# Performance work log

Hardware: AMD Instinct MI355X
Metric: run time of the kernel (lower is better)

Reference implementation:

```python
import jax, jax.numpy as jnp
import numpy as np

N_NODES = 100000
N_EDGES = 1000000
N_LABEL = 200000
D_IN = 64
D_HID = 64


def setup_inputs() -> dict:
    key = jax.random.key(0)
    ks = jax.random.split(key, 9)
    s = 1.0 / np.sqrt(D_IN)
    return {
        "x": jax.random.normal(ks[0], (N_NODES, D_IN), jnp.float32),
        "edge_index": jax.random.randint(ks[1], (2, N_EDGES), 0, N_NODES, jnp.int64),
        "edge_label_index": jax.random.randint(ks[2], (2, N_LABEL), 0, N_NODES, jnp.int64),
        "W1_l": jax.random.normal(ks[3], (D_IN, D_HID), jnp.float32) * s,
        "W1_r": jax.random.normal(ks[4], (D_IN, D_HID), jnp.float32) * s,
        "b1": jnp.zeros((D_HID,), jnp.float32),
        "W2_l": jax.random.normal(ks[5], (D_HID, D_HID), jnp.float32) * s,
        "W2_r": jax.random.normal(ks[6], (D_HID, D_HID), jnp.float32) * s,
        "b2": jnp.zeros((D_HID,), jnp.float32),
    }


def _sage_conv(x, edge_index, W_l, W_r, b):
    # PyG SAGEConv with mean aggregation: out = mean_agg @ W_l + b + x @ W_r
    src, dst = edge_index[0], edge_index[1]
    n = x.shape[0]
    # gather source features, scatter-sum into destination nodes
    agg = jax.ops.segment_sum(x[src], dst, num_segments=n)          # [N, D]
    cnt = jax.ops.segment_sum(jnp.ones(src.shape, x.dtype), dst, num_segments=n)
    mean = agg / jnp.maximum(cnt, 1.0)[:, None]
    return mean @ W_l + x @ W_r + b


def reference(x, edge_index, edge_label_index, W1_l, W1_r, b1, W2_l, W2_r, b2):
    h = jax.nn.relu(_sage_conv(x, edge_index, W1_l, W1_r, b1))
    z = _sage_conv(h, edge_index, W2_l, W2_r, b2)
    # dot-product edge decode
    src_e = z[edge_label_index[0]]  # [E_label, D]
    dst_e = z[edge_label_index[1]]
    return jnp.sum(src_e * dst_e, axis=-1)  # [E_label]
```

## Files before the change

### kernel.cpp

```cpp
#include <hip/hip_runtime.h>

#define D 64
#define NB_SHIFT 9
#define NODES_PER_B 512
#define CAP1 12288

typedef __attribute__((ext_vector_type(8))) short short8;
typedef __attribute__((ext_vector_type(4))) float f32x4;

__device__ inline unsigned short f2bf(float f) {
    unsigned int u = __float_as_uint(f);
    return (unsigned short)((u + 0x7FFFu + ((u >> 16) & 1u)) >> 16);
}
__device__ inline float bf2f(unsigned short s) {
    return __uint_as_float(((unsigned int)s) << 16);
}

__global__ void f32_to_bf16_kernel(const float* __restrict__ in,
                                   unsigned short* __restrict__ outp, int n4) {
    int i = blockIdx.x * blockDim.x + threadIdx.x;
    int stride = gridDim.x * blockDim.x;
    for (int t = i; t < n4; t += stride) {
        float4 v = ((const float4*)in)[t];
        ushort4 o;
        o.x = f2bf(v.x); o.y = f2bf(v.y); o.z = f2bf(v.z); o.w = f2bf(v.w);
        ((ushort4*)outp)[t] = o;
    }
}

__global__ __launch_bounds__(256) void bin_edges_kernel(
        const int* __restrict__ src, const int* __restrict__ dst,
        int* __restrict__ gcount, int2* __restrict__ binned,
        int n_edges, int n_buckets) {
    __shared__ int lhist[256];
    __shared__ int lbase[256];
    int tid = threadIdx.x;
    int per = (n_edges + gridDim.x - 1) / gridDim.x;
    int beg = blockIdx.x * per;
    int end = min(beg + per, n_edges);

    lhist[tid] = 0;
    __syncthreads();
    for (int e = beg + tid; e < end; e += 256)
        atomicAdd(&lhist[dst[e] >> NB_SHIFT], 1);
    __syncthreads();
    if (tid < n_buckets && lhist[tid] > 0)
        lbase[tid] = atomicAdd(&gcount[tid], lhist[tid]);
    else
        lbase[tid] = 0;
    __syncthreads();
    lhist[tid] = 0;
    __syncthreads();
    for (int e = beg + tid; e < end; e += 256) {
        int d = dst[e];
        int b = d >> NB_SHIFT;
        int off = lbase[b] + atomicAdd(&lhist[b], 1);
        if (off < CAP1)
            binned[(size_t)b * CAP1 + off] = make_int2(src[e], d);
    }
}

__global__ __launch_bounds__(256) void bucket_scan_kernel(
        const int* __restrict__ gcount, int* __restrict__ gbase,
        int* __restrict__ rowp, int n_buckets, int n_nodes, int n_edges) {
    __shared__ int tmp[256];
    int tid = threadIdx.x;
    int v = (tid < n_buckets) ? min(gcount[tid], CAP1) : 0;
    tmp[tid] = v;
    __syncthreads();
    for (int off = 1; off < 256; off <<= 1) {
        int t = 0;
        if (tid >= off) t = tmp[tid - off];
        __syncthreads();
        if (tid >= off) tmp[tid] += t;
        __syncthreads();
    }
    if (tid < n_buckets) gbase[tid] = tmp[tid] - v;
    if (tid == 0) rowp[n_nodes] = n_edges;
}

__global__ __launch_bounds__(256) void build_csr_kernel(
        const int2* __restrict__ binned, const int* __restrict__ gcount,
        const int* __restrict__ gbase, int* __restrict__ rowp,
        int* __restrict__ ssrc, int n_nodes) {
    __shared__ int lhist[NODES_PER_B];
    __shared__ int lbase[NODES_PER_B];
    __shared__ int tmp[256];
    __shared__ int stage[CAP1];

    int b        = blockIdx.x;
    int tid      = threadIdx.x;
    int nodebase = b << NB_SHIFT;
    int nlocal   = min(NODES_PER_B, n_nodes - nodebase);
    int cnt      = min(gcount[b], CAP1);
    int base     = gbase[b];
    const int2* ebuf = binned + (size_t)b * CAP1;

    lhist[tid] = 0;
    lhist[tid + 256] = 0;
    __syncthreads();
    for (int i = tid; i < cnt; i += 256)
        atomicAdd(&lhist[ebuf[i].y - nodebase], 1);
    __syncthreads();

    int a0 = lhist[2 * tid];
    int a1 = lhist[2 * tid + 1];
    tmp[tid] = a0 + a1;
    __syncthreads();
    for (int off = 1; off < 256; off <<= 1) {
        int t = 0;
        if (tid >= off) t = tmp[tid - off];
        __syncthreads();
        if (tid >= off) tmp[tid] += t;
        __syncthreads();
    }
    int excl = tmp[tid] - (a0 + a1);
    lbase[2 * tid]     = excl;
    lbase[2 * tid + 1] = excl + a0;
    __syncthreads();

    for (int j = tid; j < nlocal; j += 256)
        rowp[nodebase + j] = base + lbase[j];

    lhist[tid] = 0;
    lhist[tid + 256] = 0;
    __syncthreads();

    for (int i = tid; i < cnt; i += 256) {
        int2 e = ebuf[i];
        int ln = e.y - nodebase;
        int off = atomicAdd(&lhist[ln], 1);
        stage[lbase[ln] + off] = e.x;
    }
    __syncthreads();

    for (int i = tid; i < cnt; i += 256)
        ssrc[base + i] = stage[i];
}

__global__ void pack_w4_kernel(const float* __restrict__ W0,
                               const float* __restrict__ W1,
                               const float* __restrict__ W2,
                               const float* __restrict__ W3,
                               unsigned short* __restrict__ pw) {
    int idx = blockIdx.x * blockDim.x + threadIdx.x;
    if (idx >= 4 * 4096) return;
    int m = idx >> 12;
    int r = idx & 4095;
    const float* W = (m == 0) ? W0 : (m == 1) ? W1 : (m == 2) ? W2 : W3;
    int j    = r & 7;
    int lane = (r >> 3) & 63;
    int kk   = (r >> 9) & 1;
    int ct   = r >> 10;
    int k    = kk * 32 + ((lane >> 4) & 3) * 8 + j;
    int col  = ct * 16 + (lane & 15);
    pw[idx] = f2bf(W[k * D + col]);
}

__global__ __launch_bounds__(256) void aggregate_bf16_kernel(
        const unsigned short* __restrict__ feat,
        const int* __restrict__ row_ptr,
        const int* __restrict__ sorted_src,
        unsigned short* __restrict__ mean_out,
        int n_nodes) {
    int lane = threadIdx.x & 63;
    int r    = lane >> 4;
    int c    = lane & 15;
    int wave   = (int)((blockIdx.x * blockDim.x + threadIdx.x) >> 6);
    int nwaves = (int)((gridDim.x * blockDim.x) >> 6);

    for (int node = wave; node < n_nodes; node += nwaves) {
        int beg = row_ptr[node];
        int end = row_ptr[node + 1];
        int endm1 = end - 1;
        float a0 = 0.f, a1 = 0.f, a2 = 0.f, a3 = 0.f;

        for (int i = beg; i < end; i += 8) {
            int e0 = i + r;
            int e1 = i + 4 + r;
            int s0 = sorted_src[min(e0, endm1)];
            int s1 = sorted_src[min(e1, endm1)];
            ushort4 v0 = *(const ushort4*)(feat + ((size_t)s0 << 6) + (c << 2));
            ushort4 v1 = *(const ushort4*)(feat + ((size_t)s1 << 6) + (c << 2));
            if (e0 < end) {
                a0 += bf2f(v0.x); a1 += bf2f(v0.y);
                a2 += bf2f(v0.z); a3 += bf2f(v0.w);
            }
            if (e1 < end) {
                a0 += bf2f(v1.x); a1 += bf2f(v1.y);
                a2 += bf2f(v1.z); a3 += bf2f(v1.w);
            }
        }
        a0 += __shfl_xor(a0, 16); a1 += __shfl_xor(a1, 16);
        a2 += __shfl_xor(a2, 16); a3 += __shfl_xor(a3, 16);
        a0 += __shfl_xor(a0, 32); a1 += __shfl_xor(a1, 32);
        a2 += __shfl_xor(a2, 32); a3 += __shfl_xor(a3, 32);

        float inv = 1.0f / (float)max(end - beg, 1);
        if (r == 0) {
            ushort4 o;
            o.x = f2bf(a0 * inv); o.y = f2bf(a1 * inv);
            o.z = f2bf(a2 * inv); o.w = f2bf(a3 * inv);
            *(ushort4*)(mean_out + ((size_t)node << 6) + (c << 2)) = o;
        }
    }
}

__global__ __launch_bounds__(256) void sage_linear_mfma_kernel(
        const unsigned short* __restrict__ mean,
        const unsigned short* __restrict__ xin,
        const unsigned short* __restrict__ pwl,
        const unsigned short* __restrict__ pwr,
        const float* __restrict__ bias,
        unsigned short* __restrict__ outp,
        int n_nodes, int do_relu) {
    int lane = threadIdx.x & 63;
    int wid  = threadIdx.x >> 6;
    int arow = lane & 15;
    int kgrp = lane >> 4;

    short8 wl[4][2], wr[4][2];
#pragma unroll
    for (int ct = 0; ct < 4; ++ct)
#pragma unroll
        for (int kk = 0; kk < 2; ++kk) {
            wl[ct][kk] = *(const short8*)(pwl + (((ct * 2 + kk) * 64 + lane) << 3));
            wr[ct][kk] = *(const short8*)(pwr + (((ct * 2 + kk) * 64 + lane) << 3));
        }
    float bj[4];
#pragma unroll
    for (int ct = 0; ct < 4; ++ct) bj[ct] = bias[ct * 16 + arow];

    int wave   = blockIdx.x * 4 + wid;
    int nwaves = gridDim.x * 4;
    int ntiles = (n_nodes + 15) >> 4;

    for (int t = wave; t < ntiles; t += nwaves) {
        int base = t * 16;
        int lrow = base + arow;
        if (lrow >= n_nodes) lrow = n_nodes - 1;
        const unsigned short* mrow = mean + (size_t)lrow * D + kgrp * 8;
        const unsigned short* xrow = xin  + (size_t)lrow * D + kgrp * 8;
        short8 am0 = *(const short8*)(mrow);
        short8 am1 = *(const short8*)(mrow + 32);
        short8 ax0 = *(const short8*)(xrow);
        short8 ax1 = *(const short8*)(xrow + 32);

#pragma unroll
        for (int ct = 0; ct < 4; ++ct) {
            f32x4 acc = {0.f, 0.f, 0.f, 0.f};
            acc = __builtin_amdgcn_mfma_f32_16x16x32_bf16(am0, wl[ct][0], acc, 0, 0, 0);
            acc = __builtin_amdgcn_mfma_f32_16x16x32_bf16(am1, wl[ct][1], acc, 0, 0, 0);
            acc = __builtin_amdgcn_mfma_f32_16x16x32_bf16(ax0, wr[ct][0], acc, 0, 0, 0);
            acc = __builtin_amdgcn_mfma_f32_16x16x32_bf16(ax1, wr[ct][1], acc, 0, 0, 0);
            int col = ct * 16 + arow;
#pragma unroll
            for (int rr = 0; rr < 4; ++rr) {
                int row = base + kgrp * 4 + rr;
                float v = acc[rr] + bj[ct];
                if (do_relu) v = fmaxf(v, 0.0f);
                if (row < n_nodes) outp[(size_t)row * D + col] = f2bf(v);
            }
        }
    }
}

__global__ __launch_bounds__(256) void decode_bf16_kernel(
        const unsigned short* __restrict__ z,
        const int* __restrict__ esrc,
        const int* __restrict__ edst,
        float* __restrict__ out,
        int n) {
    int lane = threadIdx.x & 63;
    int g    = lane >> 4;
    int c    = lane & 15;
    int wave   = (int)((blockIdx.x * blockDim.x + threadIdx.x) >> 6);
    int nwaves = (int)((gridDim.x * blockDim.x) >> 6);
    int niter  = (n + 3) >> 2;

    for (int it = wave; it < niter; it += nwaves) {
        int e  = it * 4 + g;
        int ec = min(e, n - 1);
        int s  = esrc[ec];
        int d0 = edst[ec];
        ushort4 vs = *(const ushort4*)(z + ((size_t)s  << 6) + (c << 2));
        ushort4 vd = *(const ushort4*)(z + ((size_t)d0 << 6) + (c << 2));
        float p = bf2f(vs.x) * bf2f(vd.x) + bf2f(vs.y) * bf2f(vd.y) +
                  bf2f(vs.z) * bf2f(vd.z) + bf2f(vs.w) * bf2f(vd.w);
        p += __shfl_xor(p, 1);
        p += __shfl_xor(p, 2);
        p += __shfl_xor(p, 4);
        p += __shfl_xor(p, 8);
        if (c == 0 && e < n) out[e] = p;
    }
}

extern "C" void kernel_launch(void* const* d_in, const int* in_sizes, int n_in,
                              void* d_out, int out_size, void* d_ws, size_t ws_size,
                              hipStream_t stream) {
    const float* x   = (const float*)d_in[0];
    const int*   ei  = (const int*)d_in[1];
    const int*   eli = (const int*)d_in[2];
    const float* W1l = (const float*)d_in[3];
    const float* W1r = (const float*)d_in[4];
    const float* b1  = (const float*)d_in[5];
    const float* W2l = (const float*)d_in[6];
    const float* W2r = (const float*)d_in[7];
    const float* b2  = (const float*)d_in[8];
    float* out = (float*)d_out;

    const int n_nodes = in_sizes[0] / D;
    const int n_edges = in_sizes[1] / 2;
    const int n_label = in_sizes[2] / 2;
    const int n_buckets = (n_nodes + NODES_PER_B - 1) >> NB_SHIFT;

    const int* e_src = ei;
    const int* e_dst = ei + n_edges;
    const int* l_src = eli;
    const int* l_dst = eli + n_label;

    unsigned short* xb    = (unsigned short*)d_ws;
    unsigned short* meanb = xb + (size_t)n_nodes * D;
    unsigned short* h     = meanb + (size_t)n_nodes * D;
    unsigned short* z     = h + (size_t)n_nodes * D;
    int* rowp   = (int*)(z + (size_t)n_nodes * D);
    int* ssrc   = rowp + (n_nodes + 1);
    int* gcount = ssrc + n_edges + 8;
    int* gbase  = gcount + 256;
    unsigned short* pw = (unsigned short*)(gbase + 256);
    unsigned short* pw1l = pw;
    unsigned short* pw1r = pw + 4096;
    unsigned short* pw2l = pw + 8192;
    unsigned short* pw2r = pw + 12288;
    int2* binned = (int2*)h;

    dim3 blk(256);
    dim3 grd_nodes(2048);
    dim3 grd_linear(512);

    f32_to_bf16_kernel<<<grd_nodes, blk, 0, stream>>>(x, xb, n_nodes * D / 4);
    pack_w4_kernel<<<dim3(64), blk, 0, stream>>>(W1l, W1r, W2l, W2r, pw);

    hipMemsetAsync(gcount, 0, 256 * sizeof(int), stream);
    bin_edges_kernel<<<dim3(512), blk, 0, stream>>>(e_src, e_dst, gcount, binned,
                                                    n_edges, n_buckets);
    bucket_scan_kernel<<<dim3(1), blk, 0, stream>>>(gcount, gbase, rowp,
                                                    n_buckets, n_nodes, n_edges);
    build_csr_kernel<<<dim3(n_buckets), blk, 0, stream>>>(binned, gcount, gbase,
                                                          rowp, ssrc, n_nodes);

    aggregate_bf16_kernel<<<grd_nodes, blk, 0, stream>>>(xb, rowp, ssrc, meanb, n_nodes);
    sage_linear_mfma_kernel<<<grd_linear, blk, 0, stream>>>(meanb, xb, pw1l, pw1r, b1,
                                                            h, n_nodes, 1);

    aggregate_bf16_kernel<<<grd_nodes, blk, 0, stream>>>(h, rowp, ssrc, meanb, n_nodes);
    sage_linear_mfma_kernel<<<grd_linear, blk, 0, stream>>>(meanb, h, pw2l, pw2r, b2,
                                                            z, n_nodes, 0);

    decode_bf16_kernel<<<grd_nodes, blk, 0, stream>>>(z, l_src, l_dst, out, n_label);
}
```

Measured before the change: 156.4 us.

## Pack binned edges into one int, fuse bucket scan, contiguous node ranges in aggregation

Binned edges are stored as a single int (source shifted left, plus the local destination offset) instead of an int2, which halves the binning traffic. The single-block bucket scan kernel is folded into build_csr, where every block recomputes the prefix over bucket counts, removing one launch and the gbase buffer. The aggregation kernel now gives each wave a contiguous range of nodes so row_ptr is read once per node, and it unrolls the edge loop to 16 edges per iteration for more loads in flight. The packing assumes the shifted source index fits in 32 bits, and contiguous node ranges can leave waves unevenly loaded.

```diff
diff --git a/kernel.cpp b/kernel.cpp
--- a/kernel.cpp
+++ b/kernel.cpp
@@ -30,7 +30,7 @@
 
 __global__ __launch_bounds__(256) void bin_edges_kernel(
         const int* __restrict__ src, const int* __restrict__ dst,
-        int* __restrict__ gcount, int2* __restrict__ binned,
+        int* __restrict__ gcount, int* __restrict__ binned,
         int n_edges, int n_buckets) {
     __shared__ int lhist[256];
     __shared__ int lbase[256];
@@ -56,15 +56,23 @@
         int b = d >> NB_SHIFT;
         int off = lbase[b] + atomicAdd(&lhist[b], 1);
         if (off < CAP1)
-            binned[(size_t)b * CAP1 + off] = make_int2(src[e], d);
-    }
-}
-
-__global__ __launch_bounds__(256) void bucket_scan_kernel(
-        const int* __restrict__ gcount, int* __restrict__ gbase,
-        int* __restrict__ rowp, int n_buckets, int n_nodes, int n_edges) {
+            binned[(size_t)b * CAP1 + off] =
+                (src[e] << NB_SHIFT) | (d & (NODES_PER_B - 1));
+    }
+}
+
+__global__ __launch_bounds__(256) void build_csr_kernel(
+        const int* __restrict__ binned, const int* __restrict__ gcount,
+        int* __restrict__ rowp, int* __restrict__ ssrc,
+        int n_nodes, int n_buckets, int n_edges) {
+    __shared__ int lhist[NODES_PER_B];
+    __shared__ int lbase[NODES_PER_B];
     __shared__ int tmp[256];
+    __shared__ int stage[CAP1];
+
+    int b   = blockIdx.x;
     int tid = threadIdx.x;
+
     int v = (tid < n_buckets) ? min(gcount[tid], CAP1) : 0;
     tmp[tid] = v;
     __syncthreads();
@@ -75,32 +83,20 @@
         if (tid >= off) tmp[tid] += t;
         __syncthreads();
     }
-    if (tid < n_buckets) gbase[tid] = tmp[tid] - v;
-    if (tid == 0) rowp[n_nodes] = n_edges;
-}
-
-__global__ __launch_bounds__(256) void build_csr_kernel(
-        const int2* __restrict__ binned, const int* __restrict__ gcount,
-        const int* __restrict__ gbase, int* __restrict__ rowp,
-        int* __restrict__ ssrc, int n_nodes) {
-    __shared__ int lhist[NODES_PER_B];
-    __shared__ int lbase[NODES_PER_B];
-    __shared__ int tmp[256];
-    __shared__ int stage[CAP1];
-
-    int b        = blockIdx.x;
-    int tid      = threadIdx.x;
+    int base = (b == 0) ? 0 : tmp[b - 1];
+    int cnt  = min(gcount[b], CAP1);
+    if (b == 0 && tid == 0) rowp[n_nodes] = n_edges;
+    __syncthreads();
+
     int nodebase = b << NB_SHIFT;
     int nlocal   = min(NODES_PER_B, n_nodes - nodebase);
-    int cnt      = min(gcount[b], CAP1);
-    int base     = gbase[b];
-    const int2* ebuf = binned + (size_t)b * CAP1;
+    const int* ebuf = binned + (size_t)b * CAP1;
 
     lhist[tid] = 0;
     lhist[tid + 256] = 0;
     __syncthreads();
     for (int i = tid; i < cnt; i += 256)
-        atomicAdd(&lhist[ebuf[i].y - nodebase], 1);
+        atomicAdd(&lhist[ebuf[i] & (NODES_PER_B - 1)], 1);
     __syncthreads();
 
     int a0 = lhist[2 * tid];
@@ -127,10 +123,10 @@
     __syncthreads();
 
     for (int i = tid; i < cnt; i += 256) {
-        int2 e = ebuf[i];
-        int ln = e.y - nodebase;
+        int e  = ebuf[i];
+        int ln = e & (NODES_PER_B - 1);
         int off = atomicAdd(&lhist[ln], 1);
-        stage[lbase[ln] + off] = e.x;
+        stage[lbase[ln] + off] = e >> NB_SHIFT;
     }
     __syncthreads();
 
@@ -168,20 +164,27 @@
     int c    = lane & 15;
     int wave   = (int)((blockIdx.x * blockDim.x + threadIdx.x) >> 6);
     int nwaves = (int)((gridDim.x * blockDim.x) >> 6);
-
-    for (int node = wave; node < n_nodes; node += nwaves) {
-        int beg = row_ptr[node];
+    int npw  = (n_nodes + nwaves - 1) / nwaves;
+    int nbeg = wave * npw;
+    int nend = min(nbeg + npw, n_nodes);
+    if (nbeg >= nend) return;
+
+    int beg = row_ptr[nbeg];
+    for (int node = nbeg; node < nend; ++node) {
         int end = row_ptr[node + 1];
         int endm1 = end - 1;
         float a0 = 0.f, a1 = 0.f, a2 = 0.f, a3 = 0.f;
 
-        for (int i = beg; i < end; i += 8) {
-            int e0 = i + r;
-            int e1 = i + 4 + r;
+        for (int i = beg; i < end; i += 16) {
+            int e0 = i + r, e1 = i + 4 + r, e2 = i + 8 + r, e3 = i + 12 + r;
             int s0 = sorted_src[min(e0, endm1)];
             int s1 = sorted_src[min(e1, endm1)];
+            int s2 = sorted_src[min(e2, endm1)];
+            int s3 = sorted_src[min(e3, endm1)];
             ushort4 v0 = *(const ushort4*)(feat + ((size_t)s0 << 6) + (c << 2));
             ushort4 v1 = *(const ushort4*)(feat + ((size_t)s1 << 6) + (c << 2));
+            ushort4 v2 = *(const ushort4*)(feat + ((size_t)s2 << 6) + (c << 2));
+            ushort4 v3 = *(const ushort4*)(feat + ((size_t)s3 << 6) + (c << 2));
             if (e0 < end) {
                 a0 += bf2f(v0.x); a1 += bf2f(v0.y);
                 a2 += bf2f(v0.z); a3 += bf2f(v0.w);
@@ -189,6 +192,14 @@
             if (e1 < end) {
                 a0 += bf2f(v1.x); a1 += bf2f(v1.y);
                 a2 += bf2f(v1.z); a3 += bf2f(v1.w);
+            }
+            if (e2 < end) {
+                a0 += bf2f(v2.x); a1 += bf2f(v2.y);
+                a2 += bf2f(v2.z); a3 += bf2f(v2.w);
+            }
+            if (e3 < end) {
+                a0 += bf2f(v3.x); a1 += bf2f(v3.y);
+                a2 += bf2f(v3.z); a3 += bf2f(v3.w);
             }
         }
         a0 += __shfl_xor(a0, 16); a1 += __shfl_xor(a1, 16);
@@ -203,6 +214,7 @@
             o.z = f2bf(a2 * inv); o.w = f2bf(a3 * inv);
             *(ushort4*)(mean_out + ((size_t)node << 6) + (c << 2)) = o;
         }
+        beg = end;
     }
 }
 
@@ -326,13 +338,12 @@
     int* rowp   = (int*)(z + (size_t)n_nodes * D);
     int* ssrc   = rowp + (n_nodes + 1);
     int* gcount = ssrc + n_edges + 8;
-    int* gbase  = gcount + 256;
-    unsigned short* pw = (unsigned short*)(gbase + 256);
+    unsigned short* pw = (unsigned short*)(gcount + 256);
     unsigned short* pw1l = pw;
     unsigned short* pw1r = pw + 4096;
     unsigned short* pw2l = pw + 8192;
     unsigned short* pw2r = pw + 12288;
-    int2* binned = (int2*)h;
+    int* binned = (int*)h;
 
     dim3 blk(256);
     dim3 grd_nodes(2048);
@@ -344,10 +355,9 @@
     hipMemsetAsync(gcount, 0, 256 * sizeof(int), stream);
     bin_edges_kernel<<<dim3(512), blk, 0, stream>>>(e_src, e_dst, gcount, binned,
                                                     n_edges, n_buckets);
-    bucket_scan_kernel<<<dim3(1), blk, 0, stream>>>(gcount, gbase, rowp,
-                                                    n_buckets, n_nodes, n_edges);
-    build_csr_kernel<<<dim3(n_buckets), blk, 0, stream>>>(binned, gcount, gbase,
-                                                          rowp, ssrc, n_nodes);
+    build_csr_kernel<<<dim3(n_buckets), blk, 0, stream>>>(binned, gcount, rowp,
+                                                          ssrc, n_nodes,
+                                                          n_buckets, n_edges);
 
     aggregate_bf16_kernel<<<grd_nodes, blk, 0, stream>>>(xb, rowp, ssrc, meanb, n_nodes);
     sage_linear_mfma_kernel<<<grd_linear, blk, 0, stream>>>(meanb, xb, pw1l, pw1r, b1,
```

New measurement: 144.9 us. -7.3%, faster.
